# Optimization experiments

Hardware: AMD Instinct MI355X
Metric: run time of the kernel (lower is better)

## Reference

```python
import jax, jax.numpy as jnp
import numpy as np
import math

IN_FEATURES = 1024
OUT_FEATURES = 1024
GRID_SIZE = 5
SPLINE_ORDER = 3
BATCH = 4096
K = GRID_SIZE + 2 * SPLINE_ORDER  # 11 basis functions per feature


def make_grid():
    h = (1.0 - (-1.0)) / GRID_SIZE
    xx = np.arange(-SPLINE_ORDER, GRID_SIZE + SPLINE_ORDER + 1, dtype=np.float32) * h + (-1.0)
    return jnp.asarray(np.broadcast_to(xx, (IN_FEATURES, xx.shape[0])).copy())  # (in, K+1)


def setup_inputs() -> dict:
    key = jax.random.key(0)
    k1, k2, k3, k4 = jax.random.split(key, 4)
    x = jax.random.normal(k1, (BATCH, IN_FEATURES), dtype=jnp.float32)
    base_weight = jax.random.normal(k2, (OUT_FEATURES, IN_FEATURES), dtype=jnp.float32) * 0.02
    spline_weight = jax.random.normal(k3, (OUT_FEATURES, IN_FEATURES, K), dtype=jnp.float32) * 0.02
    spline_scaler = jax.random.normal(k4, (OUT_FEATURES, IN_FEATURES), dtype=jnp.float32) * 0.1
    return {"x": x, "base_weight": base_weight, "spline_weight": spline_weight,
            "spline_scaler": spline_scaler, "grid": make_grid()}


def trig_basis(x, grid):
    # x: (B, in) ; grid: (in, K+1) -> basis: (B, in, K)
    a = grid[:, :-1]                      # (in, K)
    b = grid[:, 1:]                       # (in, K)
    interval = jnp.maximum(b - a, 1e-8)
    xe = x[:, :, None]                    # (B, in, 1)
    inside = ((xe >= a) & (xe < b)).astype(x.dtype)
    trig = jnp.sin(jnp.pi * (xe - a) / interval)
    return inside * trig


def reference(x, base_weight, spline_weight, spline_scaler, grid):
    # base branch: SiLU(x) @ base_weight^T
    enm = jax.nn.silu(x) @ base_weight.T                     # (B, out)
    # spline branch: fused basis expansion + GEMM
    basis = trig_basis(x, grid)                              # (B, in, K)
    sw = spline_weight * spline_scaler[:, :, None]           # (out, in, K)
    snm = jnp.einsum('bik,oik->bo', basis, sw)               # (B, out)
    return enm + snm
```

## Files before the change

kernel.cpp:

```cpp
#include <hip/hip_runtime.h>
#include <hip/hip_bf16.h>

#define BATCH  4096
#define INF    1024
#define OUTF   1024
#define KSPL   11
#define KSPB   11264
#define SW_SCALE 1016.0f

using bf16    = __hip_bfloat16;
using short8  = __attribute__((ext_vector_type(8))) short;
using ushort8 = __attribute__((ext_vector_type(8))) unsigned short;
using f32x4   = __attribute__((ext_vector_type(4))) float;
using i32x4   = __attribute__((ext_vector_type(4))) int;
typedef unsigned long long u64;

__device__ __forceinline__ unsigned short f2bf(float f){
  union { float f; unsigned u; } a; a.f = f;
  return (unsigned short)((a.u + 0x7FFFu + ((a.u >> 16) & 1u)) >> 16);
}

__device__ __forceinline__ void llds16(const void* g, const void* l){
  __builtin_amdgcn_global_load_lds(
      (const __attribute__((address_space(1))) unsigned int*)g,
      (__attribute__((address_space(3))) unsigned int*)l, 16, 0, 0);
}

__device__ __forceinline__ void bar(){
  asm volatile("" ::: "memory");
  __builtin_amdgcn_s_barrier();
  asm volatile("" ::: "memory");
}

__device__ __forceinline__ f32x4 mfma16(short8 a, short8 b, f32x4 c){
  return __builtin_amdgcn_mfma_f32_16x16x32_bf16(a, b, c, 0, 0, 0);
}
__device__ __forceinline__ i32x4 mfma_i8(i32x4 a, i32x4 b, i32x4 c){
  return __builtin_amdgcn_mfma_i32_16x16x64_i8(a, b, c, 0, 0, 0);
}

__device__ __forceinline__ int swz(int L){ return L ^ (((L>>7)&7)<<4); }

__global__ __launch_bounds__(256) void prep(const float* __restrict__ x,
                                            const float* __restrict__ bw,
                                            const float* __restrict__ sw,
                                            const float* __restrict__ sc,
                                            bf16* __restrict__ A_sil,
                                            char* __restrict__ A_spl,
                                            bf16* __restrict__ W_b,
                                            char* __restrict__ W_s){
  const int t = threadIdx.x;
  if (blockIdx.x < 2048){
    const int gid = blockIdx.x * 256 + t;
    const int b  = gid >> 7;
    const int i0 = (gid & 127) * 8;
    const float* xr = x + (size_t)b * INF + i0;
    f32x4 p0 = *(const f32x4*)xr;
    f32x4 p1 = *(const f32x4*)(xr + 4);
    float v[8];
    #pragma unroll
    for (int j = 0; j < 4; ++j){ v[j] = p0[j]; v[4+j] = p1[j]; }
    ushort8 sl;
    int c[8], q[8];
    #pragma unroll
    for (int j = 0; j < 8; ++j){
      float xx = v[j];
      sl[j] = f2bf(xx / (1.0f + __expf(-xx)));
      float tt = (xx + 1.0f) * 2.5f;
      float fl = floorf(tt);
      c[j] = (int)fl + 3;
      q[j] = (int)rintf(__sinf(3.14159265358979f * (tt - fl)) * 127.0f);
    }
    *(ushort8*)(A_sil + (size_t)b*INF + i0) = sl;
    char* ar = A_spl + (size_t)b * KSPB + i0;
    #pragma unroll
    for (int k = 0; k < KSPL; ++k){
      u64 up = 0;
      #pragma unroll
      for (int j = 0; j < 8; ++j){
        unsigned char byte = (c[j] == k) ? (unsigned char)q[j] : (unsigned char)0;
        up |= ((u64)byte) << (8*j);
      }
      *(u64*)(ar + k*INF) = up;
    }
  } else {
    const int gid = (blockIdx.x - 2048) * 256 + t;
    const int o  = gid >> 7;
    const int i0 = (gid & 127) * 8;
    float buf[88];
    const float* sp = sw + ((size_t)o*INF + i0) * KSPL;
    #pragma unroll
    for (int qd = 0; qd < 22; ++qd)
      ((f32x4*)buf)[qd] = ((const f32x4*)sp)[qd];
    f32x4 c0 = *(const f32x4*)(sc + (size_t)o*INF + i0);
    f32x4 c1 = *(const f32x4*)(sc + (size_t)o*INF + i0 + 4);
    float scv[8];
    #pragma unroll
    for (int j = 0; j < 4; ++j){ scv[j] = c0[j]; scv[4+j] = c1[j]; }
    {
      const float* br = bw + (size_t)o*INF + i0;
      f32x4 v0 = *(const f32x4*)br;
      f32x4 v1 = *(const f32x4*)(br + 4);
      ushort8 u;
      #pragma unroll
      for (int j = 0; j < 4; ++j){ u[j] = f2bf(v0[j]); u[4+j] = f2bf(v1[j]); }
      *(ushort8*)(W_b + (size_t)o*INF + i0) = u;
    }
    char* wr = W_s + (size_t)o * KSPB + i0;
    #pragma unroll
    for (int k = 0; k < KSPL; ++k){
      u64 up = 0;
      #pragma unroll
      for (int j = 0; j < 8; ++j){
        float vv = buf[j*KSPL + k] * scv[j] * SW_SCALE;
        vv = fminf(fmaxf(vv, -127.0f), 127.0f);
        int qq = (int)rintf(vv);
        up |= ((u64)(unsigned char)(signed char)qq) << (8*j);
      }
      *(u64*)(wr + k*INF) = up;
    }
  }
}

template<int NS>
__global__ __launch_bounds__(512, 2) void gemm_i8k(const char* __restrict__ A,
                                                   const char* __restrict__ W,
                                                   short* __restrict__ Cp){
  constexpr int KSPLIT_B = KSPB / NS;
  constexpr int NG       = KSPLIT_B / 64;
  __shared__ __align__(16) char smem[131072];

  const int bid = blockIdx.x;
  const int xcd = bid & 7, local = bid >> 3;
  const int split = xcd >> 1;
  const int mt    = (xcd & 1) * 8 + (local >> 2);
  const int nt    = local & 3;
  const int bm = mt*256, bn = nt*256;

  const int t    = threadIdx.x;
  const int lane = t & 63, w = t >> 6;
  const int wr = w >> 2, wc = w & 3;
  const int r15 = lane & 15, hi = lane >> 4;

  int offA[8], offB[4];
  #pragma unroll
  for (int m = 0; m < 8; ++m){
    int L = (wr*128 + m*16 + r15)*64 + hi*16;
    offA[m] = swz(L);
  }
  #pragma unroll
  for (int n = 0; n < 4; ++n){
    int L = (wc*64 + n*16 + r15)*64 + hi*16;
    offB[n] = 16384 + swz(L);
  }

  const char* gA[2]; const char* gB[2];
  int ldsA[2], ldsB[2];
  #pragma unroll
  for (int j = 0; j < 2; ++j){
    int P = (t + j*512)*16;
    int L = swz(P);
    int row = L >> 6, inner = L & 63;
    gA[j] = A + (size_t)(bm + row)*KSPB + split*KSPLIT_B + inner;
    gB[j] = W + (size_t)(bn + row)*KSPB + split*KSPLIT_B + inner;
    ldsA[j] = j*8192 + w*1024;
    ldsB[j] = 16384 + j*8192 + w*1024;
  }

  #define STAGE(buf, tile) do{ \
    llds16(gA[0] + (tile)*64, smem + (buf)*32768 + ldsA[0]); \
    llds16(gA[1] + (tile)*64, smem + (buf)*32768 + ldsA[1]); \
    llds16(gB[0] + (tile)*64, smem + (buf)*32768 + ldsB[0]); \
    llds16(gB[1] + (tile)*64, smem + (buf)*32768 + ldsB[1]); }while(0)

  i32x4 acc[8][4] = {};
  i32x4 afA[4], afB[4], bfA[4], bfB[4];

  STAGE(0,0);
  STAGE(1,1);
  asm volatile("s_waitcnt vmcnt(4)" ::: "memory");
  bar();
  #pragma unroll
  for (int n = 0; n < 4; ++n) bfA[n] = *(const i32x4*)(smem + offB[n]);
  #pragma unroll
  for (int m = 0; m < 4; ++m) afA[m] = *(const i32x4*)(smem + offA[m]);

  #define BODY(tt, curA, curB, nxtA, nxtB) do{                                \
    const char* bp_ = smem + ((tt)&3)*32768;                                  \
    const char* bq_ = smem + (((tt)+1)&3)*32768;                              \
    if ((tt) + 2 < NG){                                                       \
      STAGE(((tt)+2)&3, (tt)+2);                                              \
      asm volatile("s_waitcnt vmcnt(4)" ::: "memory");                        \
    } else {                                                                  \
      asm volatile("s_waitcnt vmcnt(0)" ::: "memory");                        \
    }                                                                         \
    bar();                                                                    \
    i32x4 ag_[4];                                                             \
    __builtin_amdgcn_s_setprio(1);                                            \
    _Pragma("unroll")                                                         \
    for (int m = 0; m < 4; ++m){                                              \
      ag_[m] = *(const i32x4*)(bp_ + offA[4+m]);                              \
      _Pragma("unroll")                                                       \
      for (int n = 0; n < 4; ++n)                                             \
        acc[m][n] = mfma_i8(curA[m], curB[n], acc[m][n]);                     \
    }                                                                         \
    _Pragma("unroll")                                                         \
    for (int m = 0; m < 4; ++m){                                              \
      if ((tt) + 1 < NG){                                                     \
        nxtA[m] = *(const i32x4*)(bq_ + offA[m]);                             \
        nxtB[m] = *(const i32x4*)(bq_ + offB[m]);                             \
      }                                                                       \
      _Pragma("unroll")                                                       \
      for (int n = 0; n < 4; ++n)                                             \
        acc[4+m][n] = mfma_i8(ag_[m], curB[n], acc[4+m][n]);                  \
    }                                                                         \
    __builtin_amdgcn_s_setprio(0);                                            \
  }while(0)

  #pragma unroll 1
  for (int s = 0; s < NG/2; ++s){
    BODY(2*s,   afA, bfA, afB, bfB);
    BODY(2*s+1, afB, bfB, afA, bfA);
  }
  #undef BODY
  #undef STAGE

  short* outp = Cp + (size_t)split * (BATCH*OUTF);
  #pragma unroll
  for (int m = 0; m < 8; ++m){
    const int r0 = bm + wr*128 + m*16 + hi*4;
    #pragma unroll
    for (int n = 0; n < 4; ++n){
      const int cc = bn + wc*64 + n*16 + r15;
      #pragma unroll
      for (int j = 0; j < 4; ++j){
        int v = acc[m][n][j];
        v = (v >  32767) ?  32767 : v;
        v = (v < -32768) ? -32768 : v;
        outp[(size_t)(r0 + j) * OUTF + cc] = (short)v;
      }
    }
  }
}

__global__ __launch_bounds__(512, 2) void gemm_e(const bf16* __restrict__ A,
                                                 const bf16* __restrict__ W,
                                                 const short* __restrict__ Cp,
                                                 float* __restrict__ out){
  constexpr int NG = 32;
  __shared__ __align__(16) char smem[65536];

  const int bid = blockIdx.x;
  const int fin = (bid & 7) * 32 + (bid >> 3);
  const int mt = fin >> 3, nt = fin & 7;
  const int bm = mt*128, bn = nt*128;

  const int t    = threadIdx.x;
  const int lane = t & 63, w = t >> 6;
  const int wr = w >> 2, wc = w & 3;
  const int r15 = lane & 15, hi = lane >> 4;

  int offA[4], offB[2];
  #pragma unroll
  for (int m = 0; m < 4; ++m){
    int L = (wr*64 + m*16 + r15)*64 + hi*16;
    offA[m] = swz(L);
  }
  #pragma unroll
  for (int n = 0; n < 2; ++n){
    int L = (wc*32 + n*16 + r15)*64 + hi*16;
    offB[n] = 8192 + swz(L);
  }

  const char* gA; const char* gB;
  {
    int P = t*16;
    int L = swz(P);
    int row = L >> 6, inner = L & 63;
    gA = (const char*)A + (size_t)(bm + row)*2048 + inner;
    gB = (const char*)W + (size_t)(bn + row)*2048 + inner;
  }
  const int ldsA = w*1024;
  const int ldsB = 8192 + w*1024;

  #define STAGE(buf, tile) do{ \
    llds16(gA + (tile)*64, smem + (buf)*16384 + ldsA); \
    llds16(gB + (tile)*64, smem + (buf)*16384 + ldsB); }while(0)

  f32x4 acc[4][2] = {};
  short8 afA[4], afB[4], bfA[2], bfB[2];

  STAGE(0,0);
  STAGE(1,1);
  asm volatile("s_waitcnt vmcnt(2)" ::: "memory");
  bar();
  #pragma unroll
  for (int m = 0; m < 4; ++m) afA[m] = *(const short8*)(smem + offA[m]);
  #pragma unroll
  for (int n = 0; n < 2; ++n) bfA[n] = *(const short8*)(smem + offB[n]);

  #define BODY(tt, curA, curB, nxtA, nxtB) do{                                \
    const char* bq_ = smem + (((tt)+1)&3)*16384;                              \
    if ((tt) + 2 < NG){                                                       \
      STAGE(((tt)+2)&3, (tt)+2);                                              \
      asm volatile("s_waitcnt vmcnt(2)" ::: "memory");                        \
    } else {                                                                  \
      asm volatile("s_waitcnt vmcnt(0)" ::: "memory");                        \
    }                                                                         \
    bar();                                                                    \
    __builtin_amdgcn_s_setprio(1);                                            \
    _Pragma("unroll")                                                         \
    for (int m = 0; m < 4; ++m){                                              \
      if ((tt) + 1 < NG){                                                     \
        nxtA[m] = *(const short8*)(bq_ + offA[m]);                            \
        if (m < 2) nxtB[m] = *(const short8*)(bq_ + offB[m]);                 \
      }                                                                       \
      _Pragma("unroll")                                                       \
      for (int n = 0; n < 2; ++n)                                             \
        acc[m][n] = mfma16(curA[m], curB[n], acc[m][n]);                      \
    }                                                                         \
    __builtin_amdgcn_s_setprio(0);                                            \
  }while(0)

  #pragma unroll 1
  for (int s = 0; s < NG/2; ++s){
    BODY(2*s,   afA, bfA, afB, bfB);
    BODY(2*s+1, afB, bfB, afA, bfA);
  }
  #undef BODY
  #undef STAGE

  const float invP = 1.0f / (127.0f * SW_SCALE);
  const size_t NN = (size_t)BATCH * OUTF;
  #pragma unroll
  for (int m = 0; m < 4; ++m){
    const int r0 = bm + wr*64 + m*16 + hi*4;
    #pragma unroll
    for (int n = 0; n < 2; ++n){
      const int cc = bn + wc*32 + n*16 + r15;
      #pragma unroll
      for (int j = 0; j < 4; ++j){
        const size_t idx = (size_t)(r0 + j) * OUTF + cc;
        int s4 = (int)Cp[idx] + (int)Cp[NN + idx]
               + (int)Cp[2*NN + idx] + (int)Cp[3*NN + idx];
        out[idx] = acc[m][n][j] + (float)s4 * invP;
      }
    }
  }
}

__global__ __launch_bounds__(256) void fallback(const float* __restrict__ x,
    const float* __restrict__ bw, const float* __restrict__ sw,
    const float* __restrict__ sc, float* __restrict__ out){
  const int b = blockIdx.x, t = threadIdx.x;
  __shared__ float ls[INF], sg[INF];
  __shared__ int   lc[INF];
  for (int i = t; i < INF; i += 256){
    float xx = x[(size_t)b*INF + i];
    ls[i] = xx / (1.0f + __expf(-xx));
    float tt = (xx + 1.0f)*2.5f;
    float fl = floorf(tt);
    int c = (int)fl + 3;
    lc[i] = ((unsigned)c < 11u) ? c : -1;
    sg[i] = __sinf(3.14159265358979f*(tt - fl));
  }
  __syncthreads();
  for (int o = t; o < OUTF; o += 256){
    float acc = 0.f;
    const float* bwr = bw + (size_t)o*INF;
    const float* swr = sw + (size_t)o*INF*KSPL;
    const float* scr = sc + (size_t)o*INF;
    for (int i = 0; i < INF; ++i){
      acc = fmaf(ls[i], bwr[i], acc);
      int c = lc[i];
      if (c >= 0) acc = fmaf(sg[i]*scr[i], swr[i*KSPL + c], acc);
    }
    out[(size_t)b*OUTF + o] = acc;
  }
}

extern "C" void kernel_launch(void* const* d_in, const int* in_sizes, int n_in,
                              void* d_out, int out_size, void* d_ws, size_t ws_size,
                              hipStream_t stream){
  const float* x  = (const float*)d_in[0];
  const float* bw = (const float*)d_in[1];
  const float* sw = (const float*)d_in[2];
  const float* sc = (const float*)d_in[3];
  float* out = (float*)d_out;
  const size_t oAsil = 0;
  const size_t oAspl = oAsil + (size_t)BATCH*INF*2;
  const size_t oWb   = oAspl + (size_t)BATCH*KSPB;
  const size_t oWs   = oWb   + (size_t)OUTF*INF*2;
  const size_t oCp   = oWs   + (size_t)OUTF*KSPB;
  const size_t total = oCp   + (size_t)4*BATCH*OUTF*2;
  if (ws_size >= total){
    bf16*  A_sil = (bf16*)((char*)d_ws + oAsil);
    char*  A_spl = (char*)d_ws + oAspl;
    bf16*  W_b   = (bf16*)((char*)d_ws + oWb);
    char*  W_s   = (char*)d_ws + oWs;
    short* Cp    = (short*)((char*)d_ws + oCp);
    hipLaunchKernelGGL(prep, dim3(2560), dim3(256), 0, stream,
                       x, bw, sw, sc, A_sil, A_spl, W_b, W_s);
    gemm_i8k<4><<<dim3(256), dim3(512), 0, stream>>>(A_spl, W_s, Cp);
    gemm_e<<<dim3(256), dim3(512), 0, stream>>>(A_sil, W_b, Cp, out);
  } else {
    hipLaunchKernelGGL(fallback, dim3(BATCH), dim3(256), 0, stream, x, bw, sw, sc, out);
  }
}
```

Baseline: 95.50 us.

## Split int8 GEMM main loop into four barrier-separated interleaved phases

Replaces the two-tile register double-buffered loop with a single-tile loop split into four phases. Each phase issues one global-to-LDS stage load, a few LDS fragment reads and eight MFMAs, with workgroup barriers between phases. The aim is to spread memory issue evenly across the compute and to synchronise waves so their MFMA and load phases line up. The cost is many more barriers per tile and the loss of register prefetch of the next tile's fragments, so LDS read latency is exposed inside each tile.

```diff
diff --git a/kernel.cpp b/kernel.cpp
--- a/kernel.cpp
+++ b/kernel.cpp
@@ -167,63 +167,81 @@
     ldsB[j] = 16384 + j*8192 + w*1024;
   }
 
-  #define STAGE(buf, tile) do{ \
-    llds16(gA[0] + (tile)*64, smem + (buf)*32768 + ldsA[0]); \
-    llds16(gA[1] + (tile)*64, smem + (buf)*32768 + ldsA[1]); \
-    llds16(gB[0] + (tile)*64, smem + (buf)*32768 + ldsB[0]); \
-    llds16(gB[1] + (tile)*64, smem + (buf)*32768 + ldsB[1]); }while(0)
+  #define STG(j, tile, buf) do{                                              \
+    if (j == 0) llds16(gA[0] + (tile)*64, smem + (buf)*32768 + ldsA[0]);     \
+    if (j == 1) llds16(gA[1] + (tile)*64, smem + (buf)*32768 + ldsA[1]);     \
+    if (j == 2) llds16(gB[0] + (tile)*64, smem + (buf)*32768 + ldsB[0]);     \
+    if (j == 3) llds16(gB[1] + (tile)*64, smem + (buf)*32768 + ldsB[1]); }while(0)
 
   i32x4 acc[8][4] = {};
-  i32x4 afA[4], afB[4], bfA[4], bfB[4];
-
-  STAGE(0,0);
-  STAGE(1,1);
+
+  STG(0,0,0); STG(1,0,0); STG(2,0,0); STG(3,0,0);
+  STG(0,1,1); STG(1,1,1); STG(2,1,1); STG(3,1,1);
   asm volatile("s_waitcnt vmcnt(4)" ::: "memory");
   bar();
-  #pragma unroll
-  for (int n = 0; n < 4; ++n) bfA[n] = *(const i32x4*)(smem + offB[n]);
-  #pragma unroll
-  for (int m = 0; m < 4; ++m) afA[m] = *(const i32x4*)(smem + offA[m]);
-
-  #define BODY(tt, curA, curB, nxtA, nxtB) do{                                \
-    const char* bp_ = smem + ((tt)&3)*32768;                                  \
-    const char* bq_ = smem + (((tt)+1)&3)*32768;                              \
-    if ((tt) + 2 < NG){                                                       \
-      STAGE(((tt)+2)&3, (tt)+2);                                              \
-      asm volatile("s_waitcnt vmcnt(4)" ::: "memory");                        \
-    } else {                                                                  \
-      asm volatile("s_waitcnt vmcnt(0)" ::: "memory");                        \
-    }                                                                         \
-    bar();                                                                    \
-    i32x4 ag_[4];                                                             \
-    __builtin_amdgcn_s_setprio(1);                                            \
-    _Pragma("unroll")                                                         \
-    for (int m = 0; m < 4; ++m){                                              \
-      ag_[m] = *(const i32x4*)(bp_ + offA[4+m]);                              \
-      _Pragma("unroll")                                                       \
-      for (int n = 0; n < 4; ++n)                                             \
-        acc[m][n] = mfma_i8(curA[m], curB[n], acc[m][n]);                     \
-    }                                                                         \
-    _Pragma("unroll")                                                         \
-    for (int m = 0; m < 4; ++m){                                              \
-      if ((tt) + 1 < NG){                                                     \
-        nxtA[m] = *(const i32x4*)(bq_ + offA[m]);                             \
-        nxtB[m] = *(const i32x4*)(bq_ + offB[m]);                             \
-      }                                                                       \
-      _Pragma("unroll")                                                       \
-      for (int n = 0; n < 4; ++n)                                             \
-        acc[4+m][n] = mfma_i8(ag_[m], curB[n], acc[4+m][n]);                  \
-    }                                                                         \
-    __builtin_amdgcn_s_setprio(0);                                            \
-  }while(0)
 
   #pragma unroll 1
-  for (int s = 0; s < NG/2; ++s){
-    BODY(2*s,   afA, bfA, afB, bfB);
-    BODY(2*s+1, afB, bfB, afA, bfA);
-  }
-  #undef BODY
-  #undef STAGE
+  for (int tt = 0; tt < NG; ++tt){
+    const char* bp = smem + (tt&3)*32768;
+    const int sb = (tt+2)&3;
+    const bool st = (tt+2) < NG;
+    i32x4 af[4], ag[4], bf[4];
+
+    #pragma unroll
+    for (int m = 0; m < 4; ++m) af[m] = *(const i32x4*)(bp + offA[m]);
+    bf[0] = *(const i32x4*)(bp + offB[0]);
+    bf[1] = *(const i32x4*)(bp + offB[1]);
+    if (st) STG(0, tt+2, sb);
+    bar();
+    __builtin_amdgcn_s_setprio(1);
+    #pragma unroll
+    for (int m = 0; m < 4; ++m){
+      acc[m][0] = mfma_i8(af[m], bf[0], acc[m][0]);
+      acc[m][1] = mfma_i8(af[m], bf[1], acc[m][1]);
+    }
+    __builtin_amdgcn_s_setprio(0);
+    bar();
+
+    bf[2] = *(const i32x4*)(bp + offB[2]);
+    bf[3] = *(const i32x4*)(bp + offB[3]);
+    if (st) STG(1, tt+2, sb);
+    bar();
+    __builtin_amdgcn_s_setprio(1);
+    #pragma unroll
+    for (int m = 0; m < 4; ++m){
+      acc[m][2] = mfma_i8(af[m], bf[2], acc[m][2]);
+      acc[m][3] = mfma_i8(af[m], bf[3], acc[m][3]);
+    }
+    __builtin_amdgcn_s_setprio(0);
+    bar();
+
+    #pragma unroll
+    for (int m = 0; m < 4; ++m) ag[m] = *(const i32x4*)(bp + offA[4+m]);
+    if (st) STG(2, tt+2, sb);
+    bar();
+    __builtin_amdgcn_s_setprio(1);
+    #pragma unroll
+    for (int m = 0; m < 4; ++m){
+      acc[4+m][0] = mfma_i8(ag[m], bf[0], acc[4+m][0]);
+      acc[4+m][1] = mfma_i8(ag[m], bf[1], acc[4+m][1]);
+    }
+    __builtin_amdgcn_s_setprio(0);
+    bar();
+
+    if (st) STG(3, tt+2, sb);
+    if (st) asm volatile("s_waitcnt vmcnt(4)" ::: "memory");
+    else    asm volatile("s_waitcnt vmcnt(0)" ::: "memory");
+    bar();
+    __builtin_amdgcn_s_setprio(1);
+    #pragma unroll
+    for (int m = 0; m < 4; ++m){
+      acc[4+m][2] = mfma_i8(ag[m], bf[2], acc[4+m][2]);
+      acc[4+m][3] = mfma_i8(ag[m], bf[3], acc[4+m][3]);
+    }
+    __builtin_amdgcn_s_setprio(0);
+    bar();
+  }
+  #undef STG
 
   short* outp = Cp + (size_t)split * (BATCH*OUTF);
   #pragma unroll
```

Result: slower. 103.0 us (+7.8%).
